# Optimization experiments

Measured on AMD Instinct MI355X. Metric: run time of the kernel, lower is better.

The kernel has to match this reference:

```python
import jax, jax.numpy as jnp
import numpy as np


def setup_inputs() -> dict:
    key = jax.random.key(0)
    ks = jax.random.split(key, 6)
    B, N, F = 32, 2048, 64
    C1, C2, H = 32, 32, 512
    x = jax.random.normal(ks[0], (B, N, F), dtype=jnp.float32)
    a = jax.random.uniform(ks[1], (B, N, N), dtype=jnp.float32)
    W1 = jax.random.normal(ks[2], (F, C1), dtype=jnp.float32) * (1.0 / np.sqrt(F))
    b1 = jnp.zeros((C1,), dtype=jnp.float32)
    W2 = jax.random.normal(ks[3], (C1, C2), dtype=jnp.float32) * (1.0 / np.sqrt(C1))
    b2 = jnp.zeros((C2,), dtype=jnp.float32)
    Wf1 = jax.random.normal(ks[4], (C2, H), dtype=jnp.float32) * (1.0 / np.sqrt(C2))
    bf1 = jnp.zeros((H,), dtype=jnp.float32)
    Wf2 = jax.random.normal(ks[5], (H, 1), dtype=jnp.float32) * (1.0 / np.sqrt(H))
    bf2 = jnp.zeros((1,), dtype=jnp.float32)
    return {"x": x, "a": a, "W1": W1, "b1": b1, "W2": W2, "b2": b2,
            "Wf1": Wf1, "bf1": bf1, "Wf2": Wf2, "bf2": bf2}


def _gcn(x, a, W, b):
    # GCNConv batch mode: act(A @ X @ W + b); project first (cheaper: F -> C)
    xw = jnp.einsum('bnf,fc->bnc', x, W)
    return jax.nn.relu(jnp.einsum('bnm,bmc->bnc', a, xw) + b)


def reference(x, a, W1, b1, W2, b2, Wf1, bf1, Wf2, bf2):
    h = _gcn(x, a, W1, b1)          # [B,N,32]
    h = _gcn(h, a, W2, b2)          # [B,N,32]
    pooled = jnp.sum(h, axis=1)     # GlobalSumPool over nodes -> [B,32]
    h = jax.nn.relu(pooled @ Wf1 + bf1)  # [B,512]
    out = h @ Wf2 + bf2             # linear output activation -> [B,1]
    return out
```

## Files before the change

kernel.cpp:

```cpp
#include <hip/hip_runtime.h>
#include <hip/hip_bf16.h>

using bf16x8 = __attribute__((ext_vector_type(8))) short;
using f32x4  = __attribute__((ext_vector_type(4))) float;

static constexpr int NN = 2048;
static constexpr int NB = 32;
static constexpr int NC = 32;

__device__ __forceinline__ unsigned short f2bf(float f) {
    unsigned int u = __float_as_uint(f);
    u += 0x7FFFu + ((u >> 16) & 1u);
    return (unsigned short)(u >> 16);
}

template<int INCH>
__global__ void proj_kernel(const float* __restrict__ X, const float* __restrict__ W,
                            unsigned short* __restrict__ XWt)
{
    __shared__ float wlds[INCH * NC];
    const int b = blockIdx.y;
    const int m = blockIdx.x * 256 + threadIdx.x;
    for (int i = threadIdx.x; i < INCH * NC; i += 256) wlds[i] = W[i];
    __syncthreads();

    const float* xrow = X + ((size_t)b * NN + m) * INCH;
    float acc[NC];
#pragma unroll
    for (int c = 0; c < NC; ++c) acc[c] = 0.f;

    for (int f = 0; f < INCH; f += 4) {
        const float4 v = *reinterpret_cast<const float4*>(xrow + f);
        const float xv[4] = {v.x, v.y, v.z, v.w};
#pragma unroll
        for (int j = 0; j < 4; ++j) {
#pragma unroll
            for (int c = 0; c < NC; ++c)
                acc[c] += xv[j] * wlds[(f + j) * NC + c];
        }
    }

    unsigned short* outp = XWt + (size_t)b * NC * NN + m;
#pragma unroll
    for (int c = 0; c < NC; ++c) outp[(size_t)c * NN] = f2bf(acc[c]);
}

template<bool WRITE_H, bool REVK>
__global__ void gcn_gemm(const float* __restrict__ A, const unsigned short* __restrict__ Bt,
                         const float* __restrict__ bias, float* __restrict__ Hout,
                         float* __restrict__ pooled)
{
    const int b    = blockIdx.y;
    const int wave = threadIdx.x >> 6;
    const int lane = threadIdx.x & 63;
    const int lr   = lane & 15;
    const int kg   = lane >> 4;

    const int r0 = blockIdx.x * 64 + wave * 16;

    const float*          ap  = A  + ((size_t)b * NN + (r0 + lr)) * NN + kg * 8;
    const unsigned short* bp0 = Bt + ((size_t)b * NC + lr) * NN + kg * 8;
    const unsigned short* bp1 = bp0 + (size_t)16 * NN;

    f32x4 acc0 = {0.f, 0.f, 0.f, 0.f};
    f32x4 acc1 = {0.f, 0.f, 0.f, 0.f};

    union ABf { bf16x8 v; __hip_bfloat16 e[8]; };

    auto kstep = [&](int k) {
        const float4 x0 = *reinterpret_cast<const float4*>(ap + k);
        const float4 x1 = *reinterpret_cast<const float4*>(ap + k + 4);
        const bf16x8 bv0 = *reinterpret_cast<const bf16x8*>(bp0 + k);
        const bf16x8 bv1 = *reinterpret_cast<const bf16x8*>(bp1 + k);

        ABf af;
        af.e[0] = __float2bfloat16(x0.x); af.e[1] = __float2bfloat16(x0.y);
        af.e[2] = __float2bfloat16(x0.z); af.e[3] = __float2bfloat16(x0.w);
        af.e[4] = __float2bfloat16(x1.x); af.e[5] = __float2bfloat16(x1.y);
        af.e[6] = __float2bfloat16(x1.z); af.e[7] = __float2bfloat16(x1.w);

        acc0 = __builtin_amdgcn_mfma_f32_16x16x32_bf16(af.v, bv0, acc0, 0, 0, 0);
        acc1 = __builtin_amdgcn_mfma_f32_16x16x32_bf16(af.v, bv1, acc1, 0, 0, 0);
    };

    if constexpr (REVK) {
#pragma unroll 4
        for (int k = NN - 32; k >= 0; k -= 32) kstep(k);
    } else {
#pragma unroll 4
        for (int k = 0; k < NN; k += 32) kstep(k);
    }

    const float bias0 = bias[lr];
    const float bias1 = bias[lr + 16];

    if constexpr (WRITE_H) {
#pragma unroll
        for (int j = 0; j < 4; ++j) {
            const int row = r0 + kg * 4 + j;
            float* hp = Hout + ((size_t)b * NN + row) * NC;
            hp[lr]      = fmaxf(acc0[j] + bias0, 0.f);
            hp[lr + 16] = fmaxf(acc1[j] + bias1, 0.f);
        }
    } else {
        float s0 = 0.f, s1 = 0.f;
#pragma unroll
        for (int j = 0; j < 4; ++j) {
            s0 += fmaxf(acc0[j] + bias0, 0.f);
            s1 += fmaxf(acc1[j] + bias1, 0.f);
        }
        s0 += __shfl_xor(s0, 16); s0 += __shfl_xor(s0, 32);
        s1 += __shfl_xor(s1, 16); s1 += __shfl_xor(s1, 32);
        if (kg == 0) {
            atomicAdd(&pooled[b * NC + lr],      s0);
            atomicAdd(&pooled[b * NC + 16 + lr], s1);
        }
    }
}

__global__ void head_kernel(const float* __restrict__ pooled,
                            const float* __restrict__ Wf1, const float* __restrict__ bf1,
                            const float* __restrict__ Wf2, const float* __restrict__ bf2,
                            float* __restrict__ out)
{
    const int b = blockIdx.x;
    const int h = threadIdx.x;

    float dot = 0.f;
#pragma unroll
    for (int c = 0; c < NC; ++c)
        dot += pooled[b * NC + c] * Wf1[c * 512 + h];

    const float v   = fmaxf(dot + bf1[h], 0.f);
    float part      = v * Wf2[h];

#pragma unroll
    for (int off = 32; off >= 1; off >>= 1)
        part += __shfl_xor(part, off);

    __shared__ float red[8];
    if ((threadIdx.x & 63) == 0) red[threadIdx.x >> 6] = part;
    __syncthreads();
    if (threadIdx.x == 0) {
        float s = 0.f;
#pragma unroll
        for (int i = 0; i < 8; ++i) s += red[i];
        out[b] = s + bf2[0];
    }
}

extern "C" void kernel_launch(void* const* d_in, const int* in_sizes, int n_in,
                              void* d_out, int out_size, void* d_ws, size_t ws_size,
                              hipStream_t stream)
{
    const float* x   = (const float*)d_in[0];
    const float* a   = (const float*)d_in[1];
    const float* W1  = (const float*)d_in[2];
    const float* b1  = (const float*)d_in[3];
    const float* W2  = (const float*)d_in[4];
    const float* b2  = (const float*)d_in[5];
    const float* Wf1 = (const float*)d_in[6];
    const float* bf1 = (const float*)d_in[7];
    const float* Wf2 = (const float*)d_in[8];
    const float* bf2 = (const float*)d_in[9];
    float* out = (float*)d_out;

    char* ws = (char*)d_ws;
    unsigned short* xwt1 = (unsigned short*)(ws);
    float*          h1   = (float*)(ws + (4ull << 20));
    unsigned short* xwt2 = (unsigned short*)(ws + (12ull << 20));
    float*          pooled = (float*)(ws + (16ull << 20));

    hipMemsetAsync(pooled, 0, NB * NC * sizeof(float), stream);

    proj_kernel<64><<<dim3(NN / 256, NB), 256, 0, stream>>>(x, W1, xwt1);

    gcn_gemm<true, false><<<dim3(NN / 64, NB), 256, 0, stream>>>(
        a, xwt1, b1, h1, nullptr);

    proj_kernel<32><<<dim3(NN / 256, NB), 256, 0, stream>>>(h1, W2, xwt2);

    gcn_gemm<false, true><<<dim3(NN / 64, NB), 256, 0, stream>>>(
        a, xwt2, b2, nullptr, pooled);

    head_kernel<<<dim3(NB), 512, 0, stream>>>(pooled, Wf1, bf1, Wf2, bf2, out);
}
```

Baseline: 289.6 us.

## Stage GCN GEMM tiles through double-buffered swizzled LDS and fuse second projection

The GCN aggregation GEMM now loads coalesced 64x64 fp32 A tiles and bf16 B tiles into double-buffered, XOR-swizzled shared memory, prefetching the next tile into registers while MFMAs run on the current one. The first layer's epilogue applies bias and ReLU, then multiplies by W2 in LDS and writes the bf16 transposed projection directly. This removes the h1 round trip through global memory and the separate proj_kernel launch. The reversed-K traversal of the second pass, which reused the tail of A left in cache, is dropped, and the larger LDS footprint may lower occupancy.

```diff
diff --git a/kernel.cpp b/kernel.cpp
--- a/kernel.cpp
+++ b/kernel.cpp
@@ -45,69 +45,116 @@
     for (int c = 0; c < NC; ++c) outp[(size_t)c * NN] = f2bf(acc[c]);
 }
 
-template<bool WRITE_H, bool REVK>
-__global__ void gcn_gemm(const float* __restrict__ A, const unsigned short* __restrict__ Bt,
-                         const float* __restrict__ bias, float* __restrict__ Hout,
-                         float* __restrict__ pooled)
-{
+template<bool FUSE>
+__global__ __launch_bounds__(256, 4)
+void gcn_gemm_lds(const float* __restrict__ A, const unsigned short* __restrict__ Bt,
+                  const float* __restrict__ bias, const float* __restrict__ W2,
+                  unsigned short* __restrict__ XWt2, float* __restrict__ pooled)
+{
+    __shared__ float          Abuf[2][64 * 64];
+    __shared__ unsigned short Bbuf[2][32 * 64];
+
     const int b    = blockIdx.y;
-    const int wave = threadIdx.x >> 6;
-    const int lane = threadIdx.x & 63;
-    const int lr   = lane & 15;
-    const int kg   = lane >> 4;
-
-    const int r0 = blockIdx.x * 64 + wave * 16;
-
-    const float*          ap  = A  + ((size_t)b * NN + (r0 + lr)) * NN + kg * 8;
-    const unsigned short* bp0 = Bt + ((size_t)b * NC + lr) * NN + kg * 8;
-    const unsigned short* bp1 = bp0 + (size_t)16 * NN;
+    const int t    = threadIdx.x;
+    const int wave = t >> 6, lane = t & 63;
+    const int lr   = lane & 15, kg = lane >> 4;
+    const int brow = blockIdx.x * 64;
+
+    const int arow_l = t >> 4;
+    const int aseg   = (t & 15) ^ arow_l;
+    const int brows  = t >> 3;
+    const int bseg   = (t & 7) ^ (brows & 7);
+
+    const float*          Ab = A  + ((size_t)b * NN + brow) * NN;
+    const unsigned short* Bb = Bt + (size_t)b * NC * NN;
+
+    float4 areg[4]; bf16x8 breg;
+    auto ldregs = [&](int kc) {
+#pragma unroll
+        for (int i = 0; i < 4; ++i)
+            areg[i] = *reinterpret_cast<const float4*>(
+                Ab + (size_t)(i * 16 + arow_l) * NN + kc * 64 + aseg * 4);
+        breg = *reinterpret_cast<const bf16x8*>(
+                Bb + (size_t)brows * NN + kc * 64 + bseg * 8);
+    };
+    auto dswrite = [&](int buf) {
+#pragma unroll
+        for (int i = 0; i < 4; ++i)
+            *reinterpret_cast<float4*>(&Abuf[buf][(i * 256 + t) * 4]) = areg[i];
+        *reinterpret_cast<bf16x8*>(&Bbuf[buf][t * 8]) = breg;
+    };
 
     f32x4 acc0 = {0.f, 0.f, 0.f, 0.f};
     f32x4 acc1 = {0.f, 0.f, 0.f, 0.f};
-
     union ABf { bf16x8 v; __hip_bfloat16 e[8]; };
 
-    auto kstep = [&](int k) {
-        const float4 x0 = *reinterpret_cast<const float4*>(ap + k);
-        const float4 x1 = *reinterpret_cast<const float4*>(ap + k + 4);
-        const bf16x8 bv0 = *reinterpret_cast<const bf16x8*>(bp0 + k);
-        const bf16x8 bv1 = *reinterpret_cast<const bf16x8*>(bp1 + k);
-
-        ABf af;
-        af.e[0] = __float2bfloat16(x0.x); af.e[1] = __float2bfloat16(x0.y);
-        af.e[2] = __float2bfloat16(x0.z); af.e[3] = __float2bfloat16(x0.w);
-        af.e[4] = __float2bfloat16(x1.x); af.e[5] = __float2bfloat16(x1.y);
-        af.e[6] = __float2bfloat16(x1.z); af.e[7] = __float2bfloat16(x1.w);
-
-        acc0 = __builtin_amdgcn_mfma_f32_16x16x32_bf16(af.v, bv0, acc0, 0, 0, 0);
-        acc1 = __builtin_amdgcn_mfma_f32_16x16x32_bf16(af.v, bv1, acc1, 0, 0, 0);
-    };
-
-    if constexpr (REVK) {
-#pragma unroll 4
-        for (int k = NN - 32; k >= 0; k -= 32) kstep(k);
-    } else {
-#pragma unroll 4
-        for (int k = 0; k < NN; k += 32) kstep(k);
-    }
-
-    const float bias0 = bias[lr];
-    const float bias1 = bias[lr + 16];
-
-    if constexpr (WRITE_H) {
+    ldregs(0); dswrite(0); __syncthreads();
+
+    const int r = wave * 16 + lr;
+    int cur = 0;
+    for (int kc = 0; kc < NN / 64; ++kc) {
+        if (kc + 1 < NN / 64) ldregs(kc + 1);
+#pragma unroll
+        for (int k2 = 0; k2 < 2; ++k2) {
+            const int s0 = k2 * 8 + kg * 2;
+            const float4 a0 = *reinterpret_cast<const float4*>(
+                &Abuf[cur][r * 64 + ((s0    ) ^ lr) * 4]);
+            const float4 a1 = *reinterpret_cast<const float4*>(
+                &Abuf[cur][r * 64 + ((s0 + 1) ^ lr) * 4]);
+            const int sb = (k2 * 4 + kg) ^ (lr & 7);
+            const bf16x8 bv0 = *reinterpret_cast<const bf16x8*>(
+                &Bbuf[cur][lr        * 64 + sb * 8]);
+            const bf16x8 bv1 = *reinterpret_cast<const bf16x8*>(
+                &Bbuf[cur][(lr + 16) * 64 + sb * 8]);
+
+            ABf af;
+            af.e[0] = __float2bfloat16(a0.x); af.e[1] = __float2bfloat16(a0.y);
+            af.e[2] = __float2bfloat16(a0.z); af.e[3] = __float2bfloat16(a0.w);
+            af.e[4] = __float2bfloat16(a1.x); af.e[5] = __float2bfloat16(a1.y);
+            af.e[6] = __float2bfloat16(a1.z); af.e[7] = __float2bfloat16(a1.w);
+
+            acc0 = __builtin_amdgcn_mfma_f32_16x16x32_bf16(af.v, bv0, acc0, 0, 0, 0);
+            acc1 = __builtin_amdgcn_mfma_f32_16x16x32_bf16(af.v, bv1, acc1, 0, 0, 0);
+        }
+        if (kc + 1 < NN / 64) dswrite(cur ^ 1);
+        __syncthreads();
+        cur ^= 1;
+    }
+
+    const float b0  = bias[lr];
+    const float b1v = bias[lr + 16];
+
+    if constexpr (FUSE) {
+        float* hl  = &Abuf[0][0];
+        float* w2l = reinterpret_cast<float*>(&Bbuf[0][0]);
 #pragma unroll
         for (int j = 0; j < 4; ++j) {
-            const int row = r0 + kg * 4 + j;
-            float* hp = Hout + ((size_t)b * NN + row) * NC;
-            hp[lr]      = fmaxf(acc0[j] + bias0, 0.f);
-            hp[lr + 16] = fmaxf(acc1[j] + bias1, 0.f);
-        }
+            const int rr = wave * 16 + kg * 4 + j;
+            hl[rr * 33 + lr]      = fmaxf(acc0[j] + b0,  0.f);
+            hl[rr * 33 + lr + 16] = fmaxf(acc1[j] + b1v, 0.f);
+        }
+        *reinterpret_cast<float4*>(&w2l[t * 4]) =
+            *reinterpret_cast<const float4*>(&W2[t * 4]);
+        __syncthreads();
+
+        const int m  = t >> 2;
+        const int c0 = (t & 3) * 8;
+        float o[8] = {0.f, 0.f, 0.f, 0.f, 0.f, 0.f, 0.f, 0.f};
+#pragma unroll
+        for (int c = 0; c < 32; ++c) {
+            const float hv = hl[m * 33 + c];
+#pragma unroll
+            for (int i = 0; i < 8; ++i) o[i] += hv * w2l[c * 32 + c0 + i];
+        }
+        unsigned short* op = XWt2 + (size_t)b * NC * NN + brow + m;
+#pragma unroll
+        for (int i = 0; i < 8; ++i) op[(size_t)(c0 + i) * NN] = f2bf(o[i]);
     } else {
         float s0 = 0.f, s1 = 0.f;
 #pragma unroll
         for (int j = 0; j < 4; ++j) {
-            s0 += fmaxf(acc0[j] + bias0, 0.f);
-            s1 += fmaxf(acc1[j] + bias1, 0.f);
+            s0 += fmaxf(acc0[j] + b0,  0.f);
+            s1 += fmaxf(acc1[j] + b1v, 0.f);
         }
         s0 += __shfl_xor(s0, 16); s0 += __shfl_xor(s0, 32);
         s1 += __shfl_xor(s1, 16); s1 += __shfl_xor(s1, 32);
@@ -131,8 +178,8 @@
     for (int c = 0; c < NC; ++c)
         dot += pooled[b * NC + c] * Wf1[c * 512 + h];
 
-    const float v   = fmaxf(dot + bf1[h], 0.f);
-    float part      = v * Wf2[h];
+    const float v = fmaxf(dot + bf1[h], 0.f);
+    float part    = v * Wf2[h];
 
 #pragma unroll
     for (int off = 32; off >= 1; off >>= 1)
@@ -166,22 +213,19 @@
     float* out = (float*)d_out;
 
     char* ws = (char*)d_ws;
-    unsigned short* xwt1 = (unsigned short*)(ws);
-    float*          h1   = (float*)(ws + (4ull << 20));
-    unsigned short* xwt2 = (unsigned short*)(ws + (12ull << 20));
-    float*          pooled = (float*)(ws + (16ull << 20));
+    unsigned short* xwt1   = (unsigned short*)(ws);
+    unsigned short* xwt2   = (unsigned short*)(ws + (4ull << 20));
+    float*          pooled = (float*)(ws + (8ull << 20));
 
     hipMemsetAsync(pooled, 0, NB * NC * sizeof(float), stream);
 
     proj_kernel<64><<<dim3(NN / 256, NB), 256, 0, stream>>>(x, W1, xwt1);
 
-    gcn_gemm<true, false><<<dim3(NN / 64, NB), 256, 0, stream>>>(
-        a, xwt1, b1, h1, nullptr);
-
-    proj_kernel<32><<<dim3(NN / 256, NB), 256, 0, stream>>>(h1, W2, xwt2);
-
-    gcn_gemm<false, true><<<dim3(NN / 64, NB), 256, 0, stream>>>(
-        a, xwt2, b2, nullptr, pooled);
+    gcn_gemm_lds<true><<<dim3(NN / 64, NB), 256, 0, stream>>>(
+        a, xwt1, b1, W2, xwt2, nullptr);
+
+    gcn_gemm_lds<false><<<dim3(NN / 64, NB), 256, 0, stream>>>(
+        a, xwt2, b2, nullptr, nullptr, pooled);
 
     head_kernel<<<dim3(NB), 512, 0, stream>>>(pooled, Wf1, bf1, Wf2, bf2, out);
 }
```

Result: slower. 337.5 us (+16.5%).
